# Kernel tuning notes

Measured on AMD Instinct MI355X. Metric: run time of the kernel, lower is better.

Reference implementation:

```python
import jax, jax.numpy as jnp
import numpy as np

V = 1000   # vocab_size
E = 1024   # encoder_output_dim
D = 512    # decoder_hidden_dim
A = 512    # attention_hidden_dim
T = 128    # token_embedding_size
B = 128    # batch
P = 196    # num_pix (14x14)
L = 257    # latex length -> 256 decode steps


def setup_inputs() -> dict:
    key = jax.random.key(0)
    ks = jax.random.split(key, 16)
    def p(k, shape, scale=0.05):
        return (jax.random.normal(k, shape, jnp.float32) * scale)
    return dict(
        features=jax.random.normal(ks[0], (B, P, E), jnp.float32),
        latexes=jax.random.randint(ks[1], (B, L), 0, V),
        emb=p(ks[2], (V, T)),
        Wenc=p(ks[3], (A, E)), benc=jnp.zeros((A,), jnp.float32),
        Wdec=p(ks[4], (A, D)), bdec=jnp.zeros((A,), jnp.float32),
        Wattn=p(ks[5], (1, A)), battn=jnp.zeros((1,), jnp.float32),
        W1ih=p(ks[6], (4 * D, E + T)), W1hh=p(ks[7], (4 * D, D)),
        b1ih=jnp.zeros((4 * D,), jnp.float32), b1hh=jnp.zeros((4 * D,), jnp.float32),
        W2ih=p(ks[8], (4 * D, D)), W2hh=p(ks[9], (4 * D, D)),
        b2ih=jnp.zeros((4 * D,), jnp.float32), b2hh=jnp.zeros((4 * D,), jnp.float32),
        Wh0=p(ks[10], (D, E)), bh0=jnp.zeros((D,), jnp.float32),
        Wc0=p(ks[11], (D, E)), bc0=jnp.zeros((D,), jnp.float32),
        Wg=p(ks[12], (E, D)), bg=jnp.zeros((E,), jnp.float32),
        Wf=p(ks[13], (V, D)), bf=jnp.zeros((V,), jnp.float32),
    )


def _lstm_cell(x, h, c, Wih, Whh, bih, bhh):
    # torch.nn.LSTMCell: gates order i, f, g, o
    g = x @ Wih.T + bih + h @ Whh.T + bhh
    i, f, gg, o = jnp.split(g, 4, axis=1)
    c_new = jax.nn.sigmoid(f) * c + jax.nn.sigmoid(i) * jnp.tanh(gg)
    h_new = jax.nn.sigmoid(o) * jnp.tanh(c_new)
    return h_new, c_new


def reference(features, latexes, emb, Wenc, benc, Wdec, bdec, Wattn, battn,
              W1ih, W1hh, b1ih, b1hh, W2ih, W2hh, b2ih, b2hh,
              Wh0, bh0, Wc0, bc0, Wg, bg, Wf, bf):
    seq_length = latexes.shape[1] - 1
    embeds = emb[latexes]                      # [B, L, T]
    mean_enc = features.mean(axis=1)           # [B, E]
    h1 = mean_enc @ Wh0.T + bh0
    c1 = mean_enc @ Wc0.T + bc0
    h2, c2 = h1, c1
    # encoder branch of attention is step-invariant; hoist out of the loop
    enc_t = features @ Wenc.T + benc           # [B, P, A]
    wa = Wattn[0]                              # [A]
    ba = battn[0]

    def step(carry, emb_s):
        h1, c1, h2, c2 = carry
        dec_t = h2 @ Wdec.T + bdec                         # [B, A]
        attn = jnp.tanh(enc_t + dec_t[:, None, :]) @ wa + ba  # [B, P]
        alpha = jax.nn.softmax(attn, axis=1)
        awe = jnp.einsum('bp,bpe->be', alpha, features)    # [B, E]
        x1 = jnp.concatenate([emb_s, awe], axis=1)         # [B, T+E]
        # NOTE: original computes gate = sigmoid(Wg h2 + bg) and multiplies the
        # attention encoding AFTER lstm1_input was built -> dead code; omitted.
        h1n, c1n = _lstm_cell(x1, h1, c1, W1ih, W1hh, b1ih, b1hh)
        h2n, c2n = _lstm_cell(h1n, h2, c2, W2ih, W2hh, b2ih, b2hh)
        out = h2n @ Wf.T + bf                              # [B, V]
        return (h1n, c1n, h2n, c2n), (out, alpha)

    emb_seq = jnp.swapaxes(embeds[:, :seq_length], 0, 1)   # [S, B, T]
    _, (preds, alphas) = jax.lax.scan(step, (h1, c1, h2, c2), emb_seq)
    preds = jnp.swapaxes(preds, 0, 1)                      # [B, S, V]
    alphas = jnp.swapaxes(alphas, 0, 1)                    # [B, S, P]
    return preds, alphas
```

## Files before the change

### kernel.cpp

```cpp
#include <hip/hip_runtime.h>
#include <stdint.h>

#define VV 1000
#define EE 1024
#define DD 512
#define AA 512
#define TT 128
#define BB 128
#define PP 196
#define SS 256

typedef unsigned short ushort_t;
typedef unsigned long long ull_t;
typedef __attribute__((ext_vector_type(8))) short short8;
typedef __attribute__((ext_vector_type(4))) float floatx4;
typedef __attribute__((ext_vector_type(4))) unsigned short ushort4_t;
typedef __attribute__((ext_vector_type(8))) unsigned short ushort8_t;
typedef __attribute__((ext_vector_type(2))) unsigned long long ull2;

__device__ __forceinline__ float bf2f(unsigned short h) {
    return __uint_as_float(((unsigned int)h) << 16);
}
__device__ __forceinline__ unsigned short f2bf(float x) {
    unsigned int u = __float_as_uint(x);
    unsigned int r = (u + 0x7fffu + ((u >> 16) & 1u)) >> 16;
    return (unsigned short)r;
}
__device__ __forceinline__ float fast_rcp(float x) { return __builtin_amdgcn_rcpf(x); }
__device__ __forceinline__ float sigmoidf_(float x) { return fast_rcp(1.f + __expf(-x)); }
__device__ __forceinline__ float tanhf_(float x) {
    float e = __expf(2.f * x);
    return 1.f - 2.f * fast_rcp(e + 1.f);
}

__device__ __forceinline__ short8 ldA16(const ushort_t* p) {
    ull2 v;
    v.x = __hip_atomic_load((const ull_t*)p, __ATOMIC_RELAXED, __HIP_MEMORY_SCOPE_AGENT);
    v.y = __hip_atomic_load((const ull_t*)p + 1, __ATOMIC_RELAXED, __HIP_MEMORY_SCOPE_AGENT);
    return __builtin_bit_cast(short8, v);
}
__device__ __forceinline__ void stC8(ushort_t* p, ull_t v) {
    __hip_atomic_store((ull_t*)p, v, __ATOMIC_RELAXED, __HIP_MEMORY_SCOPE_AGENT);
}
__device__ __forceinline__ void stC4(ushort_t* p, unsigned int v) {
    __hip_atomic_store((unsigned int*)p, v, __ATOMIC_RELAXED, __HIP_MEMORY_SCOPE_AGENT);
}
__device__ __forceinline__ void stCf(float* p, float v) {
    __hip_atomic_store(p, v, __ATOMIC_RELAXED, __HIP_MEMORY_SCOPE_AGENT);
}
__device__ __forceinline__ float ldCf(const float* p) {
    return __hip_atomic_load(p, __ATOMIC_RELAXED, __HIP_MEMORY_SCOPE_AGENT);
}
__device__ __forceinline__ int cpoll(int* p) {
    int expected = -2000000000;
    __hip_atomic_compare_exchange_strong(p, &expected, -2000000000, __ATOMIC_RELAXED,
                                         __ATOMIC_RELAXED, __HIP_MEMORY_SCOPE_AGENT);
    return expected;
}

template <int NK, int CH>
__device__ __forceinline__ void gemm2_sc1(const ushort_t* __restrict__ ap,
                                          const ushort_t* __restrict__ bp0,
                                          const ushort_t* __restrict__ bp1,
                                          floatx4& acc0, floatx4& acc1) {
    static_assert(NK % CH == 0, "");
    constexpr int NCH = NK / CH;
    short8 ab[2][CH];
#pragma unroll
    for (int i = 0; i < CH; ++i) ab[0][i] = ldA16(ap + i * 32);
#pragma unroll
    for (int c = 0; c < NCH; ++c) {
        if (c + 1 < NCH) {
#pragma unroll
            for (int i = 0; i < CH; ++i)
                ab[(c + 1) & 1][i] = ldA16(ap + ((c + 1) * CH + i) * 32);
        }
#pragma unroll
        for (int i = 0; i < CH; ++i) {
            const int ks = c * CH + i;
            short8 b0 = *(const short8*)(bp0 + ks * 32);
            short8 b1 = *(const short8*)(bp1 + ks * 32);
            acc0 = __builtin_amdgcn_mfma_f32_16x16x32_bf16(ab[c & 1][i], b0, acc0, 0, 0, 0);
            acc1 = __builtin_amdgcn_mfma_f32_16x16x32_bf16(ab[c & 1][i], b1, acc1, 0, 0, 0);
        }
    }
}


__global__ void cvt_kernel(const float* __restrict__ src, ushort_t* __restrict__ dst, int n) {
    int i = blockIdx.x * 256 + threadIdx.x;
    if (i < n) dst[i] = f2bf(src[i]);
}

__global__ void zero_kernel(int* __restrict__ p, int n) {
    int i = blockIdx.x * 256 + threadIdx.x;
    if (i < n) p[i] = 0;
}

__global__ void addv_kernel(const float* __restrict__ a, const float* __restrict__ b,
                            float* __restrict__ o, int n) {
    int i = blockIdx.x * 256 + threadIdx.x;
    if (i < n) o[i] = a[i] + b[i];
}

__global__ void mean_kernel(const float* __restrict__ feat, float* __restrict__ meanv) {
    int idx = blockIdx.x * 256 + threadIdx.x;
    int b = idx >> 10;
    int e = idx & 1023;
    const float* p = feat + (size_t)b * PP * 1024 + e;
    float s = 0.f;
    for (int pp = 0; pp < PP; ++pp) s += p[(size_t)pp * 1024];
    meanv[idx] = s * (1.f / 196.f);
}

__global__ __launch_bounds__(256) void init_kernel(
    const float* __restrict__ meanv, const float* __restrict__ Wh0, const float* __restrict__ bh0,
    const float* __restrict__ Wc0, const float* __restrict__ bc0,
    float* __restrict__ c1, float* __restrict__ c2,
    ushort_t* __restrict__ h1b, ushort_t* __restrict__ h2b) {
    int b = blockIdx.x, t = threadIdx.x;
    __shared__ float ml[1024];
    for (int i = t; i < 1024; i += 256) ml[i] = meanv[b * 1024 + i];
    __syncthreads();
    for (int d = t; d < 512; d += 256) {
        const float4* wh = (const float4*)(Wh0 + (size_t)d * 1024);
        const float4* wc = (const float4*)(Wc0 + (size_t)d * 1024);
        float ah = bh0[d], ac = bc0[d];
        #pragma unroll 4
        for (int j = 0; j < 256; ++j) {
            float4 w = wh[j];
            ah += w.x * ml[4 * j] + w.y * ml[4 * j + 1] + w.z * ml[4 * j + 2] + w.w * ml[4 * j + 3];
        }
        #pragma unroll 4
        for (int j = 0; j < 256; ++j) {
            float4 w = wc[j];
            ac += w.x * ml[4 * j] + w.y * ml[4 * j + 1] + w.z * ml[4 * j + 2] + w.w * ml[4 * j + 3];
        }
        c1[b * 512 + d] = ac;
        c2[b * 512 + d] = ac;
        ushort_t hb = f2bf(ah);
        h1b[b * 512 + d] = hb;
        h2b[b * 512 + d] = hb;
    }
}

__global__ __launch_bounds__(256) void enc_gemm(
    const ushort_t* __restrict__ feat_bf, const ushort_t* __restrict__ wenc_bf,
    const float* __restrict__ benc, ushort_t* __restrict__ enc_bf) {
    const int t = threadIdx.x, blk = blockIdx.x;
    const int bm = (blk % 392) * 64, bn = (blk / 392) * 64;
    const int lane = t & 63, wv = t >> 6;
    const int n = lane & 15, q = lane >> 4;
    const int arow = bm + wv * 16 + n;
    const short8* ap = (const short8*)(feat_bf + (size_t)arow * 1024 + q * 8);
    const short8* bp0 = (const short8*)(wenc_bf + (size_t)(bn + 0 * 16 + n) * 1024 + q * 8);
    const short8* bp1 = (const short8*)(wenc_bf + (size_t)(bn + 1 * 16 + n) * 1024 + q * 8);
    const short8* bp2 = (const short8*)(wenc_bf + (size_t)(bn + 2 * 16 + n) * 1024 + q * 8);
    const short8* bp3 = (const short8*)(wenc_bf + (size_t)(bn + 3 * 16 + n) * 1024 + q * 8);
    floatx4 acc0 = {0.f, 0.f, 0.f, 0.f}, acc1 = acc0, acc2 = acc0, acc3 = acc0;
    for (int ks = 0; ks < 32; ++ks) {
        short8 a8 = ap[ks * 4];
        acc0 = __builtin_amdgcn_mfma_f32_16x16x32_bf16(a8, bp0[ks * 4], acc0, 0, 0, 0);
        acc1 = __builtin_amdgcn_mfma_f32_16x16x32_bf16(a8, bp1[ks * 4], acc1, 0, 0, 0);
        acc2 = __builtin_amdgcn_mfma_f32_16x16x32_bf16(a8, bp2[ks * 4], acc2, 0, 0, 0);
        acc3 = __builtin_amdgcn_mfma_f32_16x16x32_bf16(a8, bp3[ks * 4], acc3, 0, 0, 0);
    }
    #pragma unroll
    for (int r = 0; r < 4; ++r) {
        int m = bm + wv * 16 + q * 4 + r;
        int a0 = bn + n;
        enc_bf[(size_t)m * 512 + a0] = f2bf(acc0[r] + benc[a0]);
        enc_bf[(size_t)m * 512 + a0 + 16] = f2bf(acc1[r] + benc[a0 + 16]);
        enc_bf[(size_t)m * 512 + a0 + 32] = f2bf(acc2[r] + benc[a0 + 32]);
        enc_bf[(size_t)m * 512 + a0 + 48] = f2bf(acc3[r] + benc[a0 + 48]);
    }
}

__device__ __forceinline__ void gbar(int* __restrict__ bar, int k) {
    asm volatile("s_waitcnt vmcnt(0)" ::: "memory");
    __syncthreads();
    if (threadIdx.x == 0) {
        __builtin_amdgcn_fence(__ATOMIC_RELEASE, "agent");
        if (cpoll(bar + 992) == 0) {
            const int g = blockIdx.x >> 5;
            int old = __hip_atomic_fetch_add(bar + g * 32, 1, __ATOMIC_RELAXED,
                                             __HIP_MEMORY_SCOPE_AGENT);
            if (old + 1 == 32 * k) {
                int r = __hip_atomic_fetch_add(bar + 320, 1, __ATOMIC_RELAXED,
                                               __HIP_MEMORY_SCOPE_AGENT);
                if (r + 1 == 8 * k) {
                    #pragma unroll
                    for (int g2 = 0; g2 < 8; ++g2)
                        __hip_atomic_fetch_add(bar + 384 + g2 * 32, 1, __ATOMIC_RELAXED,
                                               __HIP_MEMORY_SCOPE_AGENT);
                }
            }
            int spins = 0;
            while (cpoll(bar + 384 + g * 32) < k) {
                __builtin_amdgcn_s_sleep(1);
                if (++spins > 300000) {
                    __hip_atomic_store(bar + 992, 1, __ATOMIC_RELAXED, __HIP_MEMORY_SCOPE_AGENT);
                    break;
                }
            }
        }
    }
    __syncthreads();
}

__device__ __forceinline__ void preds_tile(int w2, int s, const ushort_t* __restrict__ h2cur,
                                           const ushort_t* __restrict__ wf_bf,
                                           const float* __restrict__ bfv,
                                           float* __restrict__ out, int wv, int n, int q) {
    const int vt = w2 >> 1, mt = w2 & 1;
    const int v0 = vt * 32;
    const int m0 = mt * 64 + wv * 16;
    const int vr0 = v0 + n, vr1 = v0 + 16 + n;
    const int vc0 = vr0 < VV ? vr0 : VV - 1;
    const int vc1 = vr1 < VV ? vr1 : VV - 1;
    floatx4 acc0 = {0.f, 0.f, 0.f, 0.f}, acc1 = acc0;
    gemm2_sc1<16, 8>(h2cur + (size_t)(m0 + n) * 512 + q * 8,
                     wf_bf + (size_t)vc0 * 512 + q * 8,
                     wf_bf + (size_t)vc1 * 512 + q * 8, acc0, acc1);
    const size_t so = (size_t)(s - 1) * 1000;
    #pragma unroll
    for (int r = 0; r < 4; ++r) {
        int br = m0 + q * 4 + r;
        if (vr0 < VV) out[(size_t)br * 256000 + so + vr0] = acc0[r] + bfv[vr0];
        if (vr1 < VV) out[(size_t)br * 256000 + so + vr1] = acc1[r] + bfv[vr1];
    }
}

template <int NK1, int CH1>
__device__ __forceinline__ void lstm_phase(
    int wg, int t, int wv, int n, int q, int K1,
    const ushort_t* __restrict__ A1, const ushort_t* __restrict__ W1,
    const ushort_t* __restrict__ A2v, const ushort_t* __restrict__ W2,
    const float* __restrict__ bsum,
    float& cA, float& cB, ushort_t* __restrict__ hout, float (*glds)[65]) {
    const int mt = wg >> 5, ct = wg & 31, d0 = ct * 16;
    const int rh2 = wv & 1, ch = wv >> 1;
    const int m0 = mt * 32 + rh2 * 16;
    const int g0 = ch * 2, g1 = g0 + 1;
    floatx4 acc0 = {0.f, 0.f, 0.f, 0.f}, acc1 = acc0;
    gemm2_sc1<NK1, CH1>(A1 + (size_t)(m0 + n) * K1 + q * 8,
                        W1 + (size_t)(g0 * 512 + d0 + n) * K1 + q * 8,
                        W1 + (size_t)(g1 * 512 + d0 + n) * K1 + q * 8, acc0, acc1);
    gemm2_sc1<16, 8>(A2v + (size_t)(m0 + n) * 512 + q * 8,
                     W2 + (size_t)(g0 * 512 + d0 + n) * 512 + q * 8,
                     W2 + (size_t)(g1 * 512 + d0 + n) * 512 + q * 8, acc0, acc1);
    #pragma unroll
    for (int r = 0; r < 4; ++r) {
        glds[rh2 * 16 + q * 4 + r][g0 * 16 + n] = acc0[r];
        glds[rh2 * 16 + q * 4 + r][g1 * 16 + n] = acc1[r];
    }
    __syncthreads();
    const int bl = t >> 3, dj = (t & 7) * 2;
    const int b = mt * 32 + bl, d = d0 + dj;
    float gi0 = glds[bl][dj] + bsum[d];
    float gi1 = glds[bl][dj + 1] + bsum[d + 1];
    float gf0 = glds[bl][16 + dj] + bsum[512 + d];
    float gf1 = glds[bl][17 + dj] + bsum[512 + d + 1];
    float gg0 = glds[bl][32 + dj] + bsum[1024 + d];
    float gg1 = glds[bl][33 + dj] + bsum[1024 + d + 1];
    float go0 = glds[bl][48 + dj] + bsum[1536 + d];
    float go1 = glds[bl][49 + dj] + bsum[1536 + d + 1];
    float cn0 = sigmoidf_(gf0) * cA + sigmoidf_(gi0) * tanhf_(gg0);
    float cn1 = sigmoidf_(gf1) * cB + sigmoidf_(gi1) * tanhf_(gg1);
    cA = cn0;
    cB = cn1;
    float hn0 = sigmoidf_(go0) * tanhf_(cn0);
    float hn1 = sigmoidf_(go1) * tanhf_(cn1);
    unsigned int pk = (unsigned int)f2bf(hn0) | ((unsigned int)f2bf(hn1) << 16);
    stC4(hout + (size_t)b * 512 + d, pk);
}

__global__ __launch_bounds__(256, 1) void decode_loop(
    const ushort_t* __restrict__ enc_bf, const ushort_t* __restrict__ feat_bf,
    const ushort_t* __restrict__ wdec_bf, const ushort_t* __restrict__ wf_bf,
    const ushort_t* __restrict__ emb_bf,
    const ushort_t* __restrict__ w1ih_bf, const ushort_t* __restrict__ w1hh_bf,
    const ushort_t* __restrict__ w2ih_bf, const ushort_t* __restrict__ w2hh_bf,
    const int* __restrict__ latexes,
    const float* __restrict__ wattn, const float* __restrict__ battn,
    const float* __restrict__ bdec, const float* __restrict__ bfv,
    const float* __restrict__ b1s, const float* __restrict__ b2s,
    const float* __restrict__ c1i, const float* __restrict__ c2i,
    ushort_t* __restrict__ h1b0, ushort_t* __restrict__ h1b1,
    ushort_t* __restrict__ h2b0, ushort_t* __restrict__ h2b1,
    ushort_t* __restrict__ x1_bf, float* __restrict__ decb, float* __restrict__ alpha_g,
    float* __restrict__ out, int* __restrict__ bar) {
    const int wg = blockIdx.x, t = threadIdx.x;
    const int lane = t & 63, wv = t >> 6;
    const int n = lane & 15, q = lane >> 4;

    __shared__ float wa_lds[512];
    __shared__ float dec_lds[512];
    __shared__ float red[256];
    __shared__ float attn_lds[200];
    __shared__ float alpha_lds[200];
    __shared__ float glds[32][65];

    float c1A = 0.f, c1B = 0.f, c2A = 0.f, c2B = 0.f;
    if (wg < 128) {
        const int mt = wg >> 5, ct = wg & 31;
        const int b = mt * 32 + (t >> 3), d = ct * 16 + (t & 7) * 2;
        c1A = c1i[b * 512 + d];
        c1B = c1i[b * 512 + d + 1];
        c2A = c2i[b * 512 + d];
        c2B = c2i[b * 512 + d + 1];
        for (int i = t; i < 512; i += 256) wa_lds[i] = wattn[i];
    }

    int bc = 0;
    for (int s = 0;; ++s) {
        const ushort_t* h1cur = (s & 1) ? h1b1 : h1b0;
        const ushort_t* h2cur = (s & 1) ? h2b1 : h2b0;
        ushort_t* h1nxt = (s & 1) ? h1b0 : h1b1;
        ushort_t* h2nxt = (s & 1) ? h2b0 : h2b1;

        if (s == SS) {
            if (wg >= 128 && wg < 192) preds_tile(wg - 128, SS, h2cur, wf_bf, bfv, out, wv, n, q);
            break;
        }

        if (wg < 32) {
            const int nt = wg >> 1, mh = wg & 1;
            const int n0 = nt * 32;
            const int m0 = mh * 64 + wv * 16;
            floatx4 acc0 = {0.f, 0.f, 0.f, 0.f}, acc1 = acc0;
            gemm2_sc1<16, 8>(h2cur + (size_t)(m0 + n) * 512 + q * 8,
                             wdec_bf + (size_t)(n0 + n) * 512 + q * 8,
                             wdec_bf + (size_t)(n0 + 16 + n) * 512 + q * 8, acc0, acc1);
            const float cb0 = bdec[n0 + n], cb1 = bdec[n0 + 16 + n];
            #pragma unroll
            for (int r = 0; r < 4; ++r) {
                stCf(decb + (size_t)(m0 + q * 4 + r) * 512 + n0 + n, acc0[r] + cb0);
                stCf(decb + (size_t)(m0 + q * 4 + r) * 512 + n0 + 16 + n, acc1[r] + cb1);
            }
        }
        gbar(bar, ++bc);

        if (wg < BB) {
            const int b = wg;
            if (t < 32) {
                int tok = latexes[b * 257 + s];
                ull_t v = *(const ull_t*)(emb_bf + (size_t)tok * TT + t * 4);
                stC8(x1_bf + (size_t)b * 1152 + t * 4, v);
            }
            for (int i = t; i < 512; i += 256) dec_lds[i] = ldCf(decb + b * 512 + i);
            __syncthreads();
            for (int p = wv; p < PP; p += 4) {
                const ushort8_t ev =
                    *(const ushort8_t*)(enc_bf + ((size_t)(b * PP + p)) * 512 + lane * 8);
                float acc = 0.f;
                #pragma unroll
                for (int u = 0; u < 8; ++u) {
                    float x = bf2f(ev[u]) + dec_lds[lane * 8 + u];
                    acc += wa_lds[lane * 8 + u] * tanhf_(x);
                }
                #pragma unroll
                for (int off = 32; off > 0; off >>= 1) acc += __shfl_xor(acc, off, 64);
                if (lane == 0) attn_lds[p] = acc + battn[0];
            }
            __syncthreads();
            float logit = (t < PP) ? attn_lds[t] : -1e30f;
            red[t] = logit;
            __syncthreads();
            for (int st = 128; st > 0; st >>= 1) {
                if (t < st) red[t] = fmaxf(red[t], red[t + st]);
                __syncthreads();
            }
            float mx = red[0];
            __syncthreads();
            float e = (t < PP) ? __expf(logit - mx) : 0.f;
            red[t] = e;
            __syncthreads();
            for (int st = 128; st > 0; st >>= 1) {
                if (t < st) red[t] += red[t + st];
                __syncthreads();
            }
            float inv = fast_rcp(red[0]);
            if (t < PP) {
                float a = e * inv;
                stCf(alpha_g + b * 256 + t, a);
                out[(size_t)32768000 + (size_t)b * 50176 + (size_t)s * 196 + t] = a;
            }
        }
        gbar(bar, ++bc);

        {
            const int b3 = wg & 127, ebase = (wg >> 7) * 512;
            if (t < PP) alpha_lds[t] = ldCf(alpha_g + b3 * 256 + t);
            __syncthreads();
            const int e = ebase + t * 2;
            const ushort_t* fb = feat_bf + (size_t)b3 * PP * 1024 + e;
            float a0 = 0.f, a1 = 0.f;
            #pragma unroll 4
            for (int p = 0; p < PP; ++p) {
                unsigned int fv = *(const unsigned int*)(fb + (size_t)p * 1024);
                float av = alpha_lds[p];
                a0 += av * bf2f((unsigned short)(fv & 0xffffu));
                a1 += av * bf2f((unsigned short)(fv >> 16));
            }
            unsigned int pk = (unsigned int)f2bf(a0) | ((unsigned int)f2bf(a1) << 16);
            stC4(x1_bf + (size_t)b3 * 1152 + TT + e, pk);
        }
        gbar(bar, ++bc);

        if (wg < 128) {
            lstm_phase<36, 9>(wg, t, wv, n, q, 1152, x1_bf, w1ih_bf, h1cur, w1hh_bf,
                              b1s, c1A, c1B, h1nxt, glds);
        } else if (wg < 192 && s > 0) {
            preds_tile(wg - 128, s, h2cur, wf_bf, bfv, out, wv, n, q);
        }
        gbar(bar, ++bc);

        if (wg < 128)
            lstm_phase<16, 8>(wg, t, wv, n, q, 512, h1nxt, w2ih_bf, h2cur, w2hh_bf,
                              b2s, c2A, c2B, h2nxt, glds);
        gbar(bar, ++bc);
    }
}

extern "C" void kernel_launch(void* const* d_in, const int* in_sizes, int n_in,
                              void* d_out, int out_size, void* d_ws, size_t ws_size,
                              hipStream_t stream) {
    const float* features = (const float*)d_in[0];
    const int* latexes = (const int*)d_in[1];
    const float* emb = (const float*)d_in[2];
    const float* Wenc = (const float*)d_in[3];
    const float* benc = (const float*)d_in[4];
    const float* Wdec = (const float*)d_in[5];
    const float* bdec = (const float*)d_in[6];
    const float* Wattn = (const float*)d_in[7];
    const float* battn = (const float*)d_in[8];
    const float* W1ih = (const float*)d_in[9];
    const float* W1hh = (const float*)d_in[10];
    const float* b1ih = (const float*)d_in[11];
    const float* b1hh = (const float*)d_in[12];
    const float* W2ih = (const float*)d_in[13];
    const float* W2hh = (const float*)d_in[14];
    const float* b2ih = (const float*)d_in[15];
    const float* b2hh = (const float*)d_in[16];
    const float* Wh0 = (const float*)d_in[17];
    const float* bh0 = (const float*)d_in[18];
    const float* Wc0 = (const float*)d_in[19];
    const float* bc0 = (const float*)d_in[20];
    const float* Wf = (const float*)d_in[23];
    const float* bfv = (const float*)d_in[24];
    float* out = (float*)d_out;

    char* ws = (char*)d_ws;
    size_t off = 0;
    auto alloc = [&](size_t bytes) {
        void* p = ws + off;
        off += (bytes + 255) & ~(size_t)255;
        return p;
    };
    ushort_t* feat_bf = (ushort_t*)alloc(25690112ull * 2);
    ushort_t* enc_bf = (ushort_t*)alloc(12845056ull * 2);
    ushort_t* w1ih_bf = (ushort_t*)alloc(2359296ull * 2);
    ushort_t* w1hh_bf = (ushort_t*)alloc(1048576ull * 2);
    ushort_t* w2ih_bf = (ushort_t*)alloc(1048576ull * 2);
    ushort_t* w2hh_bf = (ushort_t*)alloc(1048576ull * 2);
    ushort_t* wf_bf = (ushort_t*)alloc(512000ull * 2);
    ushort_t* wdec_bf = (ushort_t*)alloc(262144ull * 2);
    ushort_t* wenc_bf = (ushort_t*)alloc(524288ull * 2);
    ushort_t* emb_bf = (ushort_t*)alloc(128000ull * 2);
    float* meanv = (float*)alloc(131072ull * 4);
    float* c1 = (float*)alloc(65536ull * 4);
    float* c2 = (float*)alloc(65536ull * 4);
    ushort_t* h1b0 = (ushort_t*)alloc(65536ull * 2);
    ushort_t* h1b1 = (ushort_t*)alloc(65536ull * 2);
    ushort_t* h2b0 = (ushort_t*)alloc(65536ull * 2);
    ushort_t* h2b1 = (ushort_t*)alloc(65536ull * 2);
    ushort_t* x1_bf = (ushort_t*)alloc(147456ull * 2);
    float* decb = (float*)alloc(65536ull * 4);
    float* alpha_g = (float*)alloc(32768ull * 4);
    float* b1s = (float*)alloc(2048ull * 4);
    float* b2s = (float*)alloc(2048ull * 4);
    int* bar = (int*)alloc(1024 * sizeof(int));

    auto cv = [&](const float* s, ushort_t* d, int n) {
        cvt_kernel<<<(n + 255) / 256, 256, 0, stream>>>(s, d, n);
    };
    cv(features, feat_bf, 25690112);
    cv(Wenc, wenc_bf, 524288);
    cv(W1ih, w1ih_bf, 2359296);
    cv(W1hh, w1hh_bf, 1048576);
    cv(W2ih, w2ih_bf, 1048576);
    cv(W2hh, w2hh_bf, 1048576);
    cv(Wf, wf_bf, 512000);
    cv(Wdec, wdec_bf, 262144);
    cv(emb, emb_bf, 128000);
    zero_kernel<<<4, 256, 0, stream>>>(bar, 1024);
    addv_kernel<<<8, 256, 0, stream>>>(b1ih, b1hh, b1s, 2048);
    addv_kernel<<<8, 256, 0, stream>>>(b2ih, b2hh, b2s, 2048);
    mean_kernel<<<512, 256, 0, stream>>>(features, meanv);
    init_kernel<<<128, 256, 0, stream>>>(meanv, Wh0, bh0, Wc0, bc0, c1, c2, h1b0, h2b0);
    enc_gemm<<<3136, 256, 0, stream>>>(feat_bf, wenc_bf, benc, enc_bf);

    decode_loop<<<256, 256, 0, stream>>>(
        enc_bf, feat_bf, wdec_bf, wf_bf, emb_bf, w1ih_bf, w1hh_bf, w2ih_bf, w2hh_bf,
        latexes, Wattn, battn, bdec, bfv, b1s, b2s, c1, c2,
        h1b0, h1b1, h2b0, h2b1, x1_bf, decb, alpha_g, out, bar);
}
```

Before: 32.83 ms.

## Fuse decoder projection, attention and context per batch block; cut grid barriers

Each of the 128 batch workgroups now computes its own Wdec·h2 projection with a scalar dot product, runs the attention softmax, and forms the context vector in one phase. This removes two of the five grid-wide barriers per decode step and the global round trips through decb and alpha_g. The preds tile moves into the attention phase so it overlaps that work. The grid barrier is rebuilt around leader-broadcast flags read with cache-bypassing loads instead of CAS polling, and gains an abort flag. In exchange, each batch block now does redundant per-row GEMV work (reading all of Wdec) and the whole context sum over 1024 features on its own, where previously 256 blocks shared it.

```diff
diff --git a/kernel.cpp b/kernel.cpp
--- a/kernel.cpp
+++ b/kernel.cpp
@@ -39,23 +39,25 @@
     v.y = __hip_atomic_load((const ull_t*)p + 1, __ATOMIC_RELAXED, __HIP_MEMORY_SCOPE_AGENT);
     return __builtin_bit_cast(short8, v);
 }
+__device__ __forceinline__ ull_t ldA8(const ushort_t* p) {
+    return __hip_atomic_load((const ull_t*)p, __ATOMIC_RELAXED, __HIP_MEMORY_SCOPE_AGENT);
+}
 __device__ __forceinline__ void stC8(ushort_t* p, ull_t v) {
     __hip_atomic_store((ull_t*)p, v, __ATOMIC_RELAXED, __HIP_MEMORY_SCOPE_AGENT);
 }
 __device__ __forceinline__ void stC4(ushort_t* p, unsigned int v) {
     __hip_atomic_store((unsigned int*)p, v, __ATOMIC_RELAXED, __HIP_MEMORY_SCOPE_AGENT);
 }
-__device__ __forceinline__ void stCf(float* p, float v) {
+__device__ __forceinline__ void stCi(int* p, int v) {
     __hip_atomic_store(p, v, __ATOMIC_RELAXED, __HIP_MEMORY_SCOPE_AGENT);
 }
-__device__ __forceinline__ float ldCf(const float* p) {
-    return __hip_atomic_load(p, __ATOMIC_RELAXED, __HIP_MEMORY_SCOPE_AGENT);
-}
-__device__ __forceinline__ int cpoll(int* p) {
-    int expected = -2000000000;
-    __hip_atomic_compare_exchange_strong(p, &expected, -2000000000, __ATOMIC_RELAXED,
-                                         __ATOMIC_RELAXED, __HIP_MEMORY_SCOPE_AGENT);
-    return expected;
+__device__ __forceinline__ int ld_cp(const int* p) {
+    int v;
+    asm volatile("global_load_dword %0, %1, off sc0 sc1\n\ts_waitcnt vmcnt(0)"
+                 : "=v"(v)
+                 : "v"(p)
+                 : "memory");
+    return v;
 }
 
 template <int NK, int CH>
@@ -180,29 +182,32 @@
     asm volatile("s_waitcnt vmcnt(0)" ::: "memory");
     __syncthreads();
     if (threadIdx.x == 0) {
-        __builtin_amdgcn_fence(__ATOMIC_RELEASE, "agent");
-        if (cpoll(bar + 992) == 0) {
+        if (ld_cp(bar + 384) == 0) {
             const int g = blockIdx.x >> 5;
-            int old = __hip_atomic_fetch_add(bar + g * 32, 1, __ATOMIC_RELAXED,
+            int old = __hip_atomic_fetch_add(bar + g * 16, 1, __ATOMIC_RELAXED,
                                              __HIP_MEMORY_SCOPE_AGENT);
-            if (old + 1 == 32 * k) {
-                int r = __hip_atomic_fetch_add(bar + 320, 1, __ATOMIC_RELAXED,
+            const bool leader = (old + 1 == 32 * k);
+            int* flag;
+            if (leader) {
+                int r = __hip_atomic_fetch_add(bar + 160, 1, __ATOMIC_RELAXED,
                                                __HIP_MEMORY_SCOPE_AGENT);
-                if (r + 1 == 8 * k) {
-                    #pragma unroll
-                    for (int g2 = 0; g2 < 8; ++g2)
-                        __hip_atomic_fetch_add(bar + 384 + g2 * 32, 1, __ATOMIC_RELAXED,
-                                               __HIP_MEMORY_SCOPE_AGENT);
+                if (r + 1 == 8 * k) stCi(bar + 192, k);
+                flag = bar + 192;
+            } else {
+                flag = bar + 256 + g * 16;
+            }
+            int spins = 0;
+            while (ld_cp(flag) < k) {
+                __builtin_amdgcn_s_sleep(2);
+                if (((++spins) & 255) == 0) {
+                    if (ld_cp(bar + 384) != 0) break;
+                    if (spins > 60000) {
+                        stCi(bar + 384, 1);
+                        break;
+                    }
                 }
             }
-            int spins = 0;
-            while (cpoll(bar + 384 + g * 32) < k) {
-                __builtin_amdgcn_s_sleep(1);
-                if (++spins > 300000) {
-                    __hip_atomic_store(bar + 992, 1, __ATOMIC_RELAXED, __HIP_MEMORY_SCOPE_AGENT);
-                    break;
-                }
-            }
+            if (leader) stCi(bar + 256 + g * 16, k);
         }
     }
     __syncthreads();
@@ -288,18 +293,20 @@
     const float* __restrict__ c1i, const float* __restrict__ c2i,
     ushort_t* __restrict__ h1b0, ushort_t* __restrict__ h1b1,
     ushort_t* __restrict__ h2b0, ushort_t* __restrict__ h2b1,
-    ushort_t* __restrict__ x1_bf, float* __restrict__ decb, float* __restrict__ alpha_g,
+    ushort_t* __restrict__ x1_bf,
     float* __restrict__ out, int* __restrict__ bar) {
     const int wg = blockIdx.x, t = threadIdx.x;
     const int lane = t & 63, wv = t >> 6;
     const int n = lane & 15, q = lane >> 4;
 
     __shared__ float wa_lds[512];
+    __shared__ float h2f[512];
     __shared__ float dec_lds[512];
     __shared__ float red[256];
     __shared__ float attn_lds[200];
     __shared__ float alpha_lds[200];
     __shared__ float glds[32][65];
+    __shared__ int pflag;
 
     float c1A = 0.f, c1B = 0.f, c2A = 0.f, c2B = 0.f;
     if (wg < 128) {
@@ -323,23 +330,9 @@
             if (wg >= 128 && wg < 192) preds_tile(wg - 128, SS, h2cur, wf_bf, bfv, out, wv, n, q);
             break;
         }
-
-        if (wg < 32) {
-            const int nt = wg >> 1, mh = wg & 1;
-            const int n0 = nt * 32;
-            const int m0 = mh * 64 + wv * 16;
-            floatx4 acc0 = {0.f, 0.f, 0.f, 0.f}, acc1 = acc0;
-            gemm2_sc1<16, 8>(h2cur + (size_t)(m0 + n) * 512 + q * 8,
-                             wdec_bf + (size_t)(n0 + n) * 512 + q * 8,
-                             wdec_bf + (size_t)(n0 + 16 + n) * 512 + q * 8, acc0, acc1);
-            const float cb0 = bdec[n0 + n], cb1 = bdec[n0 + 16 + n];
-            #pragma unroll
-            for (int r = 0; r < 4; ++r) {
-                stCf(decb + (size_t)(m0 + q * 4 + r) * 512 + n0 + n, acc0[r] + cb0);
-                stCf(decb + (size_t)(m0 + q * 4 + r) * 512 + n0 + 16 + n, acc1[r] + cb1);
-            }
-        }
-        gbar(bar, ++bc);
+        if (threadIdx.x == 0) pflag = ld_cp(bar + 384);
+        __syncthreads();
+        if (pflag != 0) break;
 
         if (wg < BB) {
             const int b = wg;
@@ -348,8 +341,29 @@
                 ull_t v = *(const ull_t*)(emb_bf + (size_t)tok * TT + t * 4);
                 stC8(x1_bf + (size_t)b * 1152 + t * 4, v);
             }
-            for (int i = t; i < 512; i += 256) dec_lds[i] = ldCf(decb + b * 512 + i);
-            __syncthreads();
+            if (t < 128) {
+                ull_t v = ldA8(h2cur + (size_t)b * 512 + t * 4);
+                ushort4_t u = __builtin_bit_cast(ushort4_t, v);
+                h2f[t * 4 + 0] = bf2f(u[0]);
+                h2f[t * 4 + 1] = bf2f(u[1]);
+                h2f[t * 4 + 2] = bf2f(u[2]);
+                h2f[t * 4 + 3] = bf2f(u[3]);
+            }
+            __syncthreads();
+            for (int d = t; d < 512; d += 256) {
+                const ushort8_t* wr = (const ushort8_t*)(wdec_bf + (size_t)d * 512);
+                float acc = 0.f;
+                #pragma unroll 4
+                for (int j = 0; j < 64; ++j) {
+                    ushort8_t w8 = wr[j];
+                    const float* h8 = &h2f[j * 8];
+                    #pragma unroll
+                    for (int u = 0; u < 8; ++u) acc += bf2f(w8[u]) * h8[u];
+                }
+                dec_lds[d] = acc + bdec[d];
+            }
+            __syncthreads();
+            const float ba = battn[0];
             for (int p = wv; p < PP; p += 4) {
                 const ushort8_t ev =
                     *(const ushort8_t*)(enc_bf + ((size_t)(b * PP + p)) * 512 + lane * 8);
@@ -361,7 +375,7 @@
                 }
                 #pragma unroll
                 for (int off = 32; off > 0; off >>= 1) acc += __shfl_xor(acc, off, 64);
-                if (lane == 0) attn_lds[p] = acc + battn[0];
+                if (lane == 0) attn_lds[p] = acc + ba;
             }
             __syncthreads();
             float logit = (t < PP) ? attn_lds[t] : -1e30f;
@@ -381,39 +395,34 @@
                 __syncthreads();
             }
             float inv = fast_rcp(red[0]);
+            float a = e * inv;
             if (t < PP) {
-                float a = e * inv;
-                stCf(alpha_g + b * 256 + t, a);
+                alpha_lds[t] = a;
                 out[(size_t)32768000 + (size_t)b * 50176 + (size_t)s * 196 + t] = a;
             }
-        }
-        gbar(bar, ++bc);
-
-        {
-            const int b3 = wg & 127, ebase = (wg >> 7) * 512;
-            if (t < PP) alpha_lds[t] = ldCf(alpha_g + b3 * 256 + t);
-            __syncthreads();
-            const int e = ebase + t * 2;
-            const ushort_t* fb = feat_bf + (size_t)b3 * PP * 1024 + e;
-            float a0 = 0.f, a1 = 0.f;
+            __syncthreads();
+            float a0 = 0.f, a1 = 0.f, a2 = 0.f, a3 = 0.f;
+            const int e0 = t * 4;
             #pragma unroll 4
             for (int p = 0; p < PP; ++p) {
-                unsigned int fv = *(const unsigned int*)(fb + (size_t)p * 1024);
                 float av = alpha_lds[p];
-                a0 += av * bf2f((unsigned short)(fv & 0xffffu));
-                a1 += av * bf2f((unsigned short)(fv >> 16));
-            }
-            unsigned int pk = (unsigned int)f2bf(a0) | ((unsigned int)f2bf(a1) << 16);
-            stC4(x1_bf + (size_t)b3 * 1152 + TT + e, pk);
+                ushort4_t f4 = *(const ushort4_t*)(feat_bf + ((size_t)(b * PP + p)) * 1024 + e0);
+                a0 += av * bf2f(f4[0]);
+                a1 += av * bf2f(f4[1]);
+                a2 += av * bf2f(f4[2]);
+                a3 += av * bf2f(f4[3]);
+            }
+            ull_t pk = (ull_t)f2bf(a0) | ((ull_t)f2bf(a1) << 16) |
+                       ((ull_t)f2bf(a2) << 32) | ((ull_t)f2bf(a3) << 48);
+            stC8(x1_bf + (size_t)b * 1152 + TT + e0, pk);
+        } else if (wg < 192 && s > 0) {
+            preds_tile(wg - 128, s, h2cur, wf_bf, bfv, out, wv, n, q);
         }
         gbar(bar, ++bc);
 
-        if (wg < 128) {
+        if (wg < 128)
             lstm_phase<36, 9>(wg, t, wv, n, q, 1152, x1_bf, w1ih_bf, h1cur, w1hh_bf,
                               b1s, c1A, c1B, h1nxt, glds);
-        } else if (wg < 192 && s > 0) {
-            preds_tile(wg - 128, s, h2cur, wf_bf, bfv, out, wv, n, q);
-        }
         gbar(bar, ++bc);
 
         if (wg < 128)
@@ -476,11 +485,9 @@
     ushort_t* h2b0 = (ushort_t*)alloc(65536ull * 2);
     ushort_t* h2b1 = (ushort_t*)alloc(65536ull * 2);
     ushort_t* x1_bf = (ushort_t*)alloc(147456ull * 2);
-    float* decb = (float*)alloc(65536ull * 4);
-    float* alpha_g = (float*)alloc(32768ull * 4);
     float* b1s = (float*)alloc(2048ull * 4);
     float* b2s = (float*)alloc(2048ull * 4);
-    int* bar = (int*)alloc(1024 * sizeof(int));
+    int* bar = (int*)alloc(512 * sizeof(int));
 
     auto cv = [&](const float* s, ushort_t* d, int n) {
         cvt_kernel<<<(n + 255) / 256, 256, 0, stream>>>(s, d, n);
@@ -494,7 +501,7 @@
     cv(Wf, wf_bf, 512000);
     cv(Wdec, wdec_bf, 262144);
     cv(emb, emb_bf, 128000);
-    zero_kernel<<<4, 256, 0, stream>>>(bar, 1024);
+    zero_kernel<<<2, 256, 0, stream>>>(bar, 512);
     addv_kernel<<<8, 256, 0, stream>>>(b1ih, b1hh, b1s, 2048);
     addv_kernel<<<8, 256, 0, stream>>>(b2ih, b2hh, b2s, 2048);
     mean_kernel<<<512, 256, 0, stream>>>(features, meanv);
@@ -504,5 +511,5 @@
     decode_loop<<<256, 256, 0, stream>>>(
         enc_bf, feat_bf, wdec_bf, wf_bf, emb_bf, w1ih_bf, w1hh_bf, w2ih_bf, w2hh_bf,
         latexes, Wattn, battn, bdec, bfv, b1s, b2s, c1, c2,
-        h1b0, h1b1, h2b0, h2b1, x1_bf, decb, alpha_g, out, bar);
-}
+        h1b0, h1b1, h2b0, h2b1, x1_bf, out, bar);
+}
```

New measurement: 33.89 ms. +3.2%, slower.
